# Optimization experiments

Measured on AMD Instinct MI355X. Metric: run time of the kernel, lower is better.

Reference implementation:

```python
import jax, jax.numpy as jnp
import numpy as np

B, L1, D, H = 4, 1024, 512, 16
L, R = 8192, 8
DFF = 4 * D
DH = D // H  # head dim = 32


def _ln(x, g, b, eps=1e-5):
    mu = x.mean(-1, keepdims=True)
    var = ((x - mu) ** 2).mean(-1, keepdims=True)
    return (x - mu) * jax.lax.rsqrt(var + eps) * g + b


def _mha(q_in, k_in, v_in, Wq, bq, Wk, bk, Wv, bv, Wo, bo):
    # Informer FullAttention (mask_flag=False), scale = 1/sqrt(head_dim), mix=False
    Bq, Lq, _ = q_in.shape
    S = k_in.shape[1]
    q = (q_in @ Wq.T + bq).reshape(Bq, Lq, H, DH)
    k = (k_in @ Wk.T + bk).reshape(Bq, S, H, DH)
    v = (v_in @ Wv.T + bv).reshape(Bq, S, H, DH)
    scores = jnp.einsum('blhe,bshe->bhls', q, k) * (1.0 / jnp.sqrt(jnp.float32(DH)))
    A = jax.nn.softmax(scores, axis=-1)
    out = jnp.einsum('bhls,bshd->blhd', A, v).reshape(Bq, Lq, D)
    return out @ Wo.T + bo


def _p(key, *shape):
    return jax.random.normal(key, shape, jnp.float32) * 0.02


def setup_inputs() -> dict:
    ks = jax.random.split(jax.random.key(0), 16)
    inp = {
        'x': jax.random.normal(ks[0], (B, L1, D), jnp.float32),
        'global_feat': jax.random.normal(ks[1], (B, D, L), jnp.float32),
        'conv_w': _p(ks[2], D, D), 'conv_b': jnp.zeros((D,), jnp.float32),
        'sWq': _p(ks[3], D, D), 'sbq': jnp.zeros((D,), jnp.float32),
        'sWk': _p(ks[4], D, D), 'sbk': jnp.zeros((D,), jnp.float32),
        'sWv': _p(ks[5], D, D), 'sbv': jnp.zeros((D,), jnp.float32),
        'sWo': _p(ks[6], D, D), 'sbo': jnp.zeros((D,), jnp.float32),
        'cWq': _p(ks[7], D, D), 'cbq': jnp.zeros((D,), jnp.float32),
        'cWk': _p(ks[8], D, D), 'cbk': jnp.zeros((D,), jnp.float32),
        'cWv': _p(ks[9], D, D), 'cbv': jnp.zeros((D,), jnp.float32),
        'cWo': _p(ks[10], D, D), 'cbo': jnp.zeros((D,), jnp.float32),
        'ffn_w1': _p(ks[11], DFF, D), 'ffn_b1': jnp.zeros((DFF,), jnp.float32),
        'ffn_w2': _p(ks[12], D, DFF), 'ffn_b2': jnp.zeros((D,), jnp.float32),
        'ln1_g': jnp.ones((D,), jnp.float32), 'ln1_b': jnp.zeros((D,), jnp.float32),
        'ln2_g': jnp.ones((D,), jnp.float32), 'ln2_b': jnp.zeros((D,), jnp.float32),
        'ln3_g': jnp.ones((D,), jnp.float32), 'ln3_b': jnp.zeros((D,), jnp.float32),
    }
    return inp


def reference(x, global_feat, conv_w, conv_b,
              sWq, sbq, sWk, sbk, sWv, sbv, sWo, sbo,
              cWq, cbq, cWk, cbk, cWv, cbv, cWo, cbo,
              ffn_w1, ffn_b1, ffn_w2, ffn_b2,
              ln1_g, ln1_b, ln2_g, ln2_b, ln3_g, ln3_b):
    b, c, length = global_feat.shape
    win = 2 * R  # step == window_size -> non-overlapping windows
    nw = (length - win) // win + 1
    w = global_feat[:, :, :nw * win].reshape(b, c, nw, win)
    # norm over singleton last dim == |max - min| per (b, c, window)
    stat = jnp.abs(w.max(-1) - w.min(-1))  # [B, C, NW]
    # pointwise Conv1d(512,512,1) + relu
    res = jax.nn.relu(jnp.einsum('oc,bcn->bon', conv_w, stat) + conv_b[None, :, None])
    cross = res.transpose(0, 2, 1)  # [B, NW, D] tokens for cross attention
    # EncoderLayer3: self-attn -> cross-attn -> FFN, post-LN residuals
    h = _ln(x + _mha(x, x, x, sWq, sbq, sWk, sbk, sWv, sbv, sWo, sbo), ln1_g, ln1_b)
    h = _ln(h + _mha(h, cross, cross, cWq, cbq, cWk, cbk, cWv, cbv, cWo, cbo), ln2_g, ln2_b)
    y = jax.nn.gelu(h @ ffn_w1.T + ffn_b1) @ ffn_w2.T + ffn_b2
    out = _ln(h + y, ln3_g, ln3_b)
    return out.transpose(0, 2, 1)  # [B, D, L1]
```

## Files before the change

### kernel.cpp

```cpp
#include <hip/hip_runtime.h>
#include <stdint.h>
#include <math.h>


typedef short  s16x8 __attribute__((ext_vector_type(8)));
typedef float  f32x4 __attribute__((ext_vector_type(4)));

__device__ inline unsigned short f2bf(float f) {
  uint32_t u = __builtin_bit_cast(uint32_t, f);
  u += 0x7fffu + ((u >> 16) & 1u);
  return (unsigned short)(u >> 16);
}
__device__ inline float bf2f(unsigned short h) {
  uint32_t u = ((uint32_t)h) << 16;
  return __builtin_bit_cast(float, u);
}
__device__ inline uint32_t cvtpk_bf16(float lo, float hi) {
  uint32_t r;
  asm("v_cvt_pk_bf16_f32 %0, %1, %2" : "=v"(r) : "v"(lo), "v"(hi));
  return r;
}

#define QSCALE 0.25503486611627154f

__global__ __launch_bounds__(256) void prep_kernel(
    const float* s0, const float* s1, const float* s2, const float* s3,
    const float* s4, const float* s5, const float* s6, const float* s7,
    const float* s8, const float* s9, const float* s10, const float* s11,
    unsigned short* dst,
    const float* __restrict__ gf, unsigned short* __restrict__ statT,
    const float* __restrict__ sbq, const float* __restrict__ sbk,
    const float* __restrict__ sbv, const float* __restrict__ cbk,
    const float* __restrict__ cbv, float* __restrict__ biasf) {
  const int bid = blockIdx.x;
  const int t = threadIdx.x;
  if (bid < 3200) {
    const size_t cum[13] = {0, 262144, 524288, 786432, 1048576, 1310720,
                            1572864, 1835008, 2097152, 2359296, 3407872,
                            4456448, 6553600};
    const float* srcs[12] = {s0, s1, s2, s3, s4, s5, s6, s7, s8, s9, s10, s11};
    size_t e0 = ((size_t)bid * 256 + t) * 8;
    int seg = 0;
    while (e0 >= cum[seg + 1]) ++seg;
    const float* sp = srcs[seg] + (e0 - cum[seg]);
    float4 a = *(const float4*)sp;
    float4 b = *(const float4*)(sp + 4);
    unsigned short o[8] = {f2bf(a.x), f2bf(a.y), f2bf(a.z), f2bf(a.w),
                           f2bf(b.x), f2bf(b.y), f2bf(b.z), f2bf(b.w)};
    *(uint4*)&dst[e0] = *(const uint4*)o;
  } else if (bid < 7296) {
    int gidx = (bid - 3200) * 256 + t;
    int n = gidx & 511;
    int c = (gidx >> 9) & 511;
    int b = gidx >> 18;
    const float4* p = (const float4*)(gf + ((size_t)(b * 512 + c) << 13) + n * 16);
    float4 w0 = p[0], w1 = p[1], w2 = p[2], w3 = p[3];
    float mx = w0.x, mn = w0.x;
    float vals[15] = {w0.y, w0.z, w0.w, w1.x, w1.y, w1.z, w1.w,
                      w2.x, w2.y, w2.z, w2.w, w3.x, w3.y, w3.z, w3.w};
#pragma unroll
    for (int i = 0; i < 15; ++i) {
      mx = fmaxf(mx, vals[i]);
      mn = fminf(mn, vals[i]);
    }
    statT[((size_t)(b * 512 + n) << 9) + c] = f2bf(mx - mn);
  } else {
    for (int i = t; i < 2560; i += 256) {
      float v;
      if (i < 512) v = sbq[i];
      else if (i < 1024) v = sbk[i - 512];
      else if (i < 1536) v = sbv[i - 1024];
      else if (i < 2048) v = cbk[i - 1536];
      else v = cbv[i - 2048];
      biasf[i] = v;
    }
  }
}

template <int ACT, int OUTBF, int SCALEQ, int BN>
__global__ __launch_bounds__(256) void gemm_bf16(
    const unsigned short* __restrict__ A, const unsigned short* __restrict__ W,
    const float* __restrict__ bias, void* __restrict__ Cout,
    int M, int N, int K) {
  constexpr int NFR = BN / 32;
  __shared__ __align__(16) unsigned short As[2][64 * 64];
  __shared__ __align__(16) unsigned short Bs[2][BN * 64];
  const int t = threadIdx.x;
  const int w = t >> 6, lane = t & 63;
  const int r = lane & 15, g = lane >> 4;
  const int wm = w >> 1, wn = w & 1;
  const int m0 = blockIdx.y * 64, n0 = blockIdx.x * BN;

  auto STAGE = [&](int buf, int k0) {
#pragma unroll
    for (int ii = 0; ii < 2; ++ii) {
      int c = t + 256 * ii;
      int row = c >> 3, sc = c & 7;
      const unsigned short* ga =
          A + (size_t)(m0 + row) * K + k0 + ((sc ^ (row & 7)) << 3);
      __builtin_amdgcn_global_load_lds(
          (const __attribute__((address_space(1))) uint32_t*)ga,
          (__attribute__((address_space(3))) uint32_t*)&As[buf][c * 8], 16, 0, 0);
    }
#pragma unroll
    for (int ii = 0; ii < BN / 32; ++ii) {
      int c = t + 256 * ii;
      int row = c >> 3, sc = c & 7;
      const unsigned short* gb =
          W + (size_t)(n0 + row) * K + k0 + ((sc ^ (row & 7)) << 3);
      __builtin_amdgcn_global_load_lds(
          (const __attribute__((address_space(1))) uint32_t*)gb,
          (__attribute__((address_space(3))) uint32_t*)&Bs[buf][c * 8], 16, 0, 0);
    }
  };

  f32x4 acc[2][NFR];
#pragma unroll
  for (int mi = 0; mi < 2; ++mi)
#pragma unroll
    for (int ni = 0; ni < NFR; ++ni) acc[mi][ni] = (f32x4){0.f, 0.f, 0.f, 0.f};

  STAGE(0, 0);
  __syncthreads();
  int cur = 0;
  for (int k0 = 0; k0 < K; k0 += 64) {
    if (k0 + 64 < K) STAGE(cur ^ 1, k0 + 64);
#pragma unroll
    for (int ks = 0; ks < 2; ++ks) {
      s16x8 af[2], bf[NFR];
#pragma unroll
      for (int mi = 0; mi < 2; ++mi)
        af[mi] = *(const s16x8*)&As[cur][(wm * 32 + mi * 16 + r) * 64 +
                                         (((ks * 4 + g) ^ (r & 7)) << 3)];
#pragma unroll
      for (int ni = 0; ni < NFR; ++ni)
        bf[ni] = *(const s16x8*)&Bs[cur][(wn * (BN / 2) + ni * 16 + r) * 64 +
                                         (((ks * 4 + g) ^ (r & 7)) << 3)];
#pragma unroll
      for (int mi = 0; mi < 2; ++mi)
#pragma unroll
        for (int ni = 0; ni < NFR; ++ni)
          acc[mi][ni] = __builtin_amdgcn_mfma_f32_16x16x32_bf16(
              af[mi], bf[ni], acc[mi][ni], 0, 0, 0);
    }
    __syncthreads();
    cur ^= 1;
  }

#pragma unroll
  for (int ni = 0; ni < NFR; ++ni) {
    const int col = n0 + wn * (BN / 2) + ni * 16 + r;
    const float bv = bias[col];
#pragma unroll
    for (int mi = 0; mi < 2; ++mi) {
#pragma unroll
      for (int rg = 0; rg < 4; ++rg) {
        const int row = m0 + wm * 32 + mi * 16 + g * 4 + rg;
        float v = acc[mi][ni][rg] + bv;
        if (ACT == 1) v = fmaxf(v, 0.f);
        if (ACT == 2) {
          float u = 0.7978845608028654f * (v + 0.044715f * v * v * v);
          float e = __expf(2.f * u);
          float th = 1.f - 2.f / (e + 1.f);
          v = 0.5f * v * (1.f + th);
        }
        if (SCALEQ && col < 512) v *= QSCALE;
        if (OUTBF)
          ((unsigned short*)Cout)[(size_t)row * N + col] = f2bf(v);
        else
          ((float*)Cout)[(size_t)row * N + col] = v;
      }
    }
  }
}

template <int S>
__global__ __launch_bounds__(512) void attn_mfma(
    const unsigned short* __restrict__ Q, int qstride,
    const unsigned short* __restrict__ K, int kstride,
    const unsigned short* __restrict__ V, int vstride,
    unsigned short* __restrict__ O) {
  constexpr int NT = S / 128;
  __shared__ __align__(16) unsigned short Kl[128 * 40];
  __shared__ __align__(16) unsigned short Vl[32 * 136];
  __shared__ __align__(16) unsigned short Pl[8][16 * 136];
  const int t = threadIdx.x;
  const int w = t >> 6, lane = t & 63;
  const int r = lane & 15, g = lane >> 4;
  const int qt = blockIdx.x, h = blockIdx.y, b = blockIdx.z;
  const int q0 = qt * 128 + w * 16;
  const int kvr = t >> 2, dsg = t & 3;

  s16x8 qa = *(const s16x8*)&Q[((size_t)(b * 1024 + q0 + r)) * qstride + h * 32 + g * 8];

  f32x4 o0 = (f32x4){0.f, 0.f, 0.f, 0.f};
  f32x4 o1 = (f32x4){0.f, 0.f, 0.f, 0.f};
  float m = -1e30f, l = 0.f;

  uint4 kA = {}, vA = {}, kB = {}, vB = {};
  auto GLOAD = [&](int nt, uint4& kr, uint4& vr) {
    const int kv0 = nt * 128;
    kr = *(const uint4*)&K[((size_t)(b * S + kv0 + kvr)) * kstride + h * 32 + dsg * 8];
    vr = *(const uint4*)&V[((size_t)(b * S + kv0 + kvr)) * vstride + h * 32 + dsg * 8];
  };
  GLOAD(0, kA, vA);

  for (int nt = 0; nt < NT; ++nt) {
    __syncthreads();
    *(uint4*)&Kl[kvr * 40 + dsg * 8] = kA;
    {
      unsigned short vs[8];
      *(uint4*)vs = vA;
#pragma unroll
      for (int u = 0; u < 8; ++u) Vl[(dsg * 8 + u) * 136 + kvr] = vs[u];
    }
    if (nt + 1 < NT) GLOAD(nt + 1, kB, vB);
    __syncthreads();

    f32x4 s[8];
    __builtin_amdgcn_s_setprio(1);
#pragma unroll
    for (int nb = 0; nb < 8; ++nb) {
      s16x8 ka = *(const s16x8*)&Kl[(nb * 16 + r) * 40 + g * 8];
      s[nb] = __builtin_amdgcn_mfma_f32_16x16x32_bf16(
          ka, qa, (f32x4){0.f, 0.f, 0.f, 0.f}, 0, 0, 0);
    }
    __builtin_amdgcn_s_setprio(0);

    float tm = -1e30f;
#pragma unroll
    for (int nb = 0; nb < 8; ++nb) {
      float a01 = fmaxf(s[nb][0], s[nb][1]);
      float a23 = fmaxf(s[nb][2], s[nb][3]);
      tm = fmaxf(tm, fmaxf(a01, a23));
    }
    tm = fmaxf(tm, __shfl_xor(tm, 16));
    tm = fmaxf(tm, __shfl_xor(tm, 32));
    const float mnew = fmaxf(m, tm);
    const float corr = __builtin_amdgcn_exp2f(m - mnew);
    float ps = 0.f;
#pragma unroll
    for (int nb = 0; nb < 8; ++nb) {
      float p0 = __builtin_amdgcn_exp2f(s[nb][0] - mnew);
      float p1 = __builtin_amdgcn_exp2f(s[nb][1] - mnew);
      float p2 = __builtin_amdgcn_exp2f(s[nb][2] - mnew);
      float p3 = __builtin_amdgcn_exp2f(s[nb][3] - mnew);
      ps += (p0 + p1) + (p2 + p3);
      uint2 pv;
      pv.x = cvtpk_bf16(p0, p1);
      pv.y = cvtpk_bf16(p2, p3);
      *(uint2*)&Pl[w][r * 136 + nb * 16 + g * 4] = pv;
    }
    ps += __shfl_xor(ps, 16);
    ps += __shfl_xor(ps, 32);
    l = l * corr + ps;
    m = mnew;
#pragma unroll
    for (int rg = 0; rg < 4; ++rg) { o0[rg] *= corr; o1[rg] *= corr; }

    __builtin_amdgcn_s_setprio(1);
#pragma unroll
    for (int ks = 0; ks < 4; ++ks) {
      s16x8 va0 = *(const s16x8*)&Vl[r * 136 + ks * 32 + g * 8];
      s16x8 va1 = *(const s16x8*)&Vl[(16 + r) * 136 + ks * 32 + g * 8];
      s16x8 pb  = *(const s16x8*)&Pl[w][r * 136 + ks * 32 + g * 8];
      o0 = __builtin_amdgcn_mfma_f32_16x16x32_bf16(va0, pb, o0, 0, 0, 0);
      o1 = __builtin_amdgcn_mfma_f32_16x16x32_bf16(va1, pb, o1, 0, 0, 0);
    }
    __builtin_amdgcn_s_setprio(0);
    kA = kB; vA = vB;
  }

  const float inv = 1.f / l;
  const size_t row = (size_t)(b * 1024 + q0 + r);
  uint2 w0, w1;
  w0.x = cvtpk_bf16(o0[0] * inv, o0[1] * inv);
  w0.y = cvtpk_bf16(o0[2] * inv, o0[3] * inv);
  w1.x = cvtpk_bf16(o1[0] * inv, o1[1] * inv);
  w1.y = cvtpk_bf16(o1[2] * inv, o1[3] * inv);
  *(uint2*)&O[row * 512 + h * 32 + g * 4]      = w0;
  *(uint2*)&O[row * 512 + h * 32 + 16 + g * 4] = w1;
}

template <int XBF, int ABF>
__global__ __launch_bounds__(256) void ln_kernel(
    const void* __restrict__ X, const void* __restrict__ A,
    const float* __restrict__ gw, const float* __restrict__ bw,
    unsigned short* __restrict__ O) {
  const int rr = blockIdx.x;
  const int t = threadIdx.x;
  const size_t base = (size_t)rr * 512;
  float x0, x1, a0, a1;
  if (XBF) {
    x0 = bf2f(((const unsigned short*)X)[base + t]);
    x1 = bf2f(((const unsigned short*)X)[base + t + 256]);
  } else {
    x0 = ((const float*)X)[base + t];
    x1 = ((const float*)X)[base + t + 256];
  }
  if (ABF) {
    a0 = bf2f(((const unsigned short*)A)[base + t]);
    a1 = bf2f(((const unsigned short*)A)[base + t + 256]);
  } else {
    a0 = ((const float*)A)[base + t];
    a1 = ((const float*)A)[base + t + 256];
  }
  float v0 = x0 + a0;
  float v1 = x1 + a1;
  __shared__ float wsum[4];
  float s = v0 + v1;
#pragma unroll
  for (int of = 32; of; of >>= 1) s += __shfl_down(s, of);
  if ((t & 63) == 0) wsum[t >> 6] = s;
  __syncthreads();
  const float mean = (wsum[0] + wsum[1] + wsum[2] + wsum[3]) * (1.f / 512.f);
  __syncthreads();
  float d0 = v0 - mean, d1 = v1 - mean;
  float s2 = d0 * d0 + d1 * d1;
#pragma unroll
  for (int of = 32; of; of >>= 1) s2 += __shfl_down(s2, of);
  if ((t & 63) == 0) wsum[t >> 6] = s2;
  __syncthreads();
  const float var = (wsum[0] + wsum[1] + wsum[2] + wsum[3]) * (1.f / 512.f);
  const float rstd = rsqrtf(var + 1e-5f);
  O[base + t] = f2bf(d0 * rstd * gw[t] + bw[t]);
  O[base + t + 256] = f2bf(d1 * rstd * gw[t + 256] + bw[t + 256]);
}

__global__ __launch_bounds__(256) void transpose_out_kernel(
    const unsigned short* __restrict__ h3, float* __restrict__ out) {
  __shared__ float tile[64][65];
  const int t = threadIdx.x;
  const int lt = blockIdx.x * 64, ct = blockIdx.y * 64, b = blockIdx.z;
#pragma unroll
  for (int ii = 0; ii < 2; ++ii) {
    int idx = t + 256 * ii;
    int row = idx >> 3, ch = idx & 7;
    uint4 v = *(const uint4*)&h3[((size_t)(b * 1024 + lt + row)) * 512 + ct + ch * 8];
    unsigned short vs[8];
    *(uint4*)vs = v;
#pragma unroll
    for (int u = 0; u < 8; ++u) tile[row][ch * 8 + u] = bf2f(vs[u]);
  }
  __syncthreads();
  const int c = t >> 2, l0 = (t & 3) * 16;
  float* op = &out[((size_t)(b * 512 + ct + c)) * 1024 + lt + l0];
#pragma unroll
  for (int i = 0; i < 4; ++i) {
    float4 o4 = {tile[l0 + i * 4 + 0][c], tile[l0 + i * 4 + 1][c],
                 tile[l0 + i * 4 + 2][c], tile[l0 + i * 4 + 3][c]};
    *(float4*)(op + i * 4) = o4;
  }
}

extern "C" void kernel_launch(void* const* d_in, const int* in_sizes, int n_in,
                              void* d_out, int out_size, void* d_ws, size_t ws_size,
                              hipStream_t stream) {
  const float* x      = (const float*)d_in[0];
  const float* gf     = (const float*)d_in[1];
  const float* conv_w = (const float*)d_in[2];
  const float* conv_b = (const float*)d_in[3];
  const float* sWq = (const float*)d_in[4],  *sbq = (const float*)d_in[5];
  const float* sWk = (const float*)d_in[6],  *sbk = (const float*)d_in[7];
  const float* sWv = (const float*)d_in[8],  *sbv = (const float*)d_in[9];
  const float* sWo = (const float*)d_in[10], *sbo = (const float*)d_in[11];
  const float* cWq = (const float*)d_in[12], *cbq = (const float*)d_in[13];
  const float* cWk = (const float*)d_in[14], *cbk = (const float*)d_in[15];
  const float* cWv = (const float*)d_in[16], *cbv = (const float*)d_in[17];
  const float* cWo = (const float*)d_in[18], *cbo = (const float*)d_in[19];
  const float* fw1 = (const float*)d_in[20], *fb1 = (const float*)d_in[21];
  const float* fw2 = (const float*)d_in[22], *fb2 = (const float*)d_in[23];
  const float* ln1_g = (const float*)d_in[24], *ln1_b = (const float*)d_in[25];
  const float* ln2_g = (const float*)d_in[26], *ln2_b = (const float*)d_in[27];
  const float* ln3_g = (const float*)d_in[28], *ln3_b = (const float*)d_in[29];
  float* out = (float*)d_out;

  unsigned short* bfp = (unsigned short*)d_ws;
  unsigned short* conv_wb = bfp + 0;
  unsigned short* sWqb = bfp + 262144;
  unsigned short* cWqb = bfp + 1310720;
  unsigned short* cWkb = bfp + 1572864;
  unsigned short* cWob = bfp + 2097152;
  unsigned short* sWob = bfp + 1048576;
  unsigned short* fw1b = bfp + 2359296, *fw2b = bfp + 3407872;
  unsigned short* xbf  = bfp + 4456448;

  unsigned short* SC   = bfp + 6553600;
  unsigned short* qkvb = SC;
  unsigned short* ckvb = SC + 6291456;
  unsigned short* qcb  = SC + 8388608;
  unsigned short* ctxb = SC + 12582912;
  unsigned short* projb= SC + 14680064;
  unsigned short* hbf  = SC + 16777216;
  unsigned short* h2bf = SC + 18874368;
  unsigned short* statTb = qcb;
  unsigned short* crossb = ctxb;
  unsigned short* midb   = qkvb;
  float* biasf = (float*)projb;

  prep_kernel<<<7297, 256, 0, stream>>>(
      conv_w, sWq, sWk, sWv, sWo, cWq, cWk, cWv, cWo, fw1, fw2, x, bfp,
      gf, statTb, sbq, sbk, sbv, cbk, cbv, biasf);

  gemm_bf16<1, 1, 0, 64><<<dim3(8, 32), 256, 0, stream>>>(
      statTb, conv_wb, conv_b, crossb, 2048, 512, 512);
  gemm_bf16<0, 1, 1, 128><<<dim3(12, 64), 256, 0, stream>>>(
      xbf, sWqb, biasf, qkvb, 4096, 1536, 512);
  gemm_bf16<0, 1, 0, 64><<<dim3(16, 32), 256, 0, stream>>>(
      crossb, cWkb, biasf + 1536, ckvb, 2048, 1024, 512);

  attn_mfma<1024><<<dim3(8, 16, 4), 512, 0, stream>>>(
      qkvb, 1536, qkvb + 512, 1536, qkvb + 1024, 1536, ctxb);
  gemm_bf16<0, 1, 0, 64><<<dim3(8, 64), 256, 0, stream>>>(
      ctxb, sWob, sbo, projb, 4096, 512, 512);
  ln_kernel<0, 1><<<4096, 256, 0, stream>>>(x, projb, ln1_g, ln1_b, hbf);

  gemm_bf16<0, 1, 1, 64><<<dim3(8, 64), 256, 0, stream>>>(
      hbf, cWqb, cbq, qcb, 4096, 512, 512);
  attn_mfma<512><<<dim3(8, 16, 4), 512, 0, stream>>>(
      qcb, 512, ckvb, 1024, ckvb + 512, 1024, ctxb);
  gemm_bf16<0, 1, 0, 64><<<dim3(8, 64), 256, 0, stream>>>(
      ctxb, cWob, cbo, projb, 4096, 512, 512);
  ln_kernel<1, 1><<<4096, 256, 0, stream>>>(hbf, projb, ln2_g, ln2_b, h2bf);

  gemm_bf16<2, 1, 0, 128><<<dim3(16, 64), 256, 0, stream>>>(
      h2bf, fw1b, fb1, midb, 4096, 2048, 512);
  gemm_bf16<0, 1, 0, 64><<<dim3(8, 64), 256, 0, stream>>>(
      midb, fw2b, fb2, projb, 4096, 512, 2048);
  ln_kernel<1, 1><<<4096, 256, 0, stream>>>(h2bf, projb, ln3_g, ln3_b, hbf);
  transpose_out_kernel<<<dim3(16, 8, 4), 256, 0, stream>>>(hbf, out);
}
```

Baseline: 335.5 us.

## Add 128x128 GEMM tile body and merge conv and QKV GEMM launches

Adds a 128x128-tile bf16 MFMA GEMM body with K-step 32 and double-buffered direct-to-LDS loads. It is used in a new combined kernel that runs the conv projection GEMM and the QKV projection GEMM in one grid by splitting on block index, and also for the FFN first layer. The larger tiles are meant to raise data reuse per block and cut one kernel launch. In exchange there are fewer blocks, which can lower occupancy and leave parts of the GPU idle, and the K-step of 32 means more synchronisations per GEMM.

```diff
diff --git a/kernel.cpp b/kernel.cpp
--- a/kernel.cpp
+++ b/kernel.cpp
@@ -77,6 +77,118 @@
   }
 }
 
+__device__ __forceinline__ void gemm128_body(
+    unsigned short* AsB, unsigned short* BsB,
+    const unsigned short* __restrict__ A, const unsigned short* __restrict__ W,
+    const float* __restrict__ bias, unsigned short* __restrict__ Cout,
+    int M, int N, int K, int m0, int n0, int act, int scaleq) {
+  const int t = threadIdx.x;
+  const int w = t >> 6, lane = t & 63;
+  const int r = lane & 15, g = lane >> 4;
+  const int wm = w >> 1, wn = w & 1;
+
+  auto STAGE = [&](int buf, int k0) {
+    unsigned short* As = AsB + buf * (128 * 32);
+    unsigned short* Bs = BsB + buf * (128 * 32);
+#pragma unroll
+    for (int ii = 0; ii < 2; ++ii) {
+      int c = t + 256 * ii;
+      int row = c >> 2, sc = c & 3;
+      const unsigned short* ga = A + (size_t)(m0 + row) * K + k0 + sc * 8;
+      __builtin_amdgcn_global_load_lds(
+          (const __attribute__((address_space(1))) uint32_t*)ga,
+          (__attribute__((address_space(3))) uint32_t*)&As[c * 8], 16, 0, 0);
+      const unsigned short* gb = W + (size_t)(n0 + row) * K + k0 + sc * 8;
+      __builtin_amdgcn_global_load_lds(
+          (const __attribute__((address_space(1))) uint32_t*)gb,
+          (__attribute__((address_space(3))) uint32_t*)&Bs[c * 8], 16, 0, 0);
+    }
+  };
+
+  f32x4 acc[4][4];
+#pragma unroll
+  for (int mi = 0; mi < 4; ++mi)
+#pragma unroll
+    for (int ni = 0; ni < 4; ++ni) acc[mi][ni] = (f32x4){0.f, 0.f, 0.f, 0.f};
+
+  STAGE(0, 0);
+  __syncthreads();
+  int cur = 0;
+  for (int k0 = 0; k0 < K; k0 += 32) {
+    if (k0 + 32 < K) STAGE(cur ^ 1, k0 + 32);
+    const unsigned short* As = AsB + cur * (128 * 32);
+    const unsigned short* Bs = BsB + cur * (128 * 32);
+    s16x8 af[4], bf[4];
+#pragma unroll
+    for (int mi = 0; mi < 4; ++mi)
+      af[mi] = *(const s16x8*)&As[(wm * 64 + mi * 16 + r) * 32 + g * 8];
+#pragma unroll
+    for (int ni = 0; ni < 4; ++ni)
+      bf[ni] = *(const s16x8*)&Bs[(wn * 64 + ni * 16 + r) * 32 + g * 8];
+#pragma unroll
+    for (int mi = 0; mi < 4; ++mi)
+#pragma unroll
+      for (int ni = 0; ni < 4; ++ni)
+        acc[mi][ni] = __builtin_amdgcn_mfma_f32_16x16x32_bf16(
+            af[mi], bf[ni], acc[mi][ni], 0, 0, 0);
+    __syncthreads();
+    cur ^= 1;
+  }
+
+#pragma unroll
+  for (int ni = 0; ni < 4; ++ni) {
+    const int col = n0 + wn * 64 + ni * 16 + r;
+    const float bv = bias[col];
+#pragma unroll
+    for (int mi = 0; mi < 4; ++mi) {
+#pragma unroll
+      for (int rg = 0; rg < 4; ++rg) {
+        const int row = m0 + wm * 64 + mi * 16 + g * 4 + rg;
+        float v = acc[mi][ni][rg] + bv;
+        if (act == 1) v = fmaxf(v, 0.f);
+        if (act == 2) {
+          float u = 0.7978845608028654f * (v + 0.044715f * v * v * v);
+          float e = __expf(2.f * u);
+          float th = 1.f - 2.f / (e + 1.f);
+          v = 0.5f * v * (1.f + th);
+        }
+        if (scaleq && col < 512) v *= QSCALE;
+        Cout[(size_t)row * N + col] = f2bf(v);
+      }
+    }
+  }
+}
+
+__global__ __launch_bounds__(256) void gemm_conv_qkv(
+    const unsigned short* __restrict__ statT,
+    const unsigned short* __restrict__ convW, const float* __restrict__ convB,
+    unsigned short* __restrict__ cross,
+    const unsigned short* __restrict__ xbf,
+    const unsigned short* __restrict__ qkvW, const float* __restrict__ qkvBias,
+    unsigned short* __restrict__ qkv) {
+  __shared__ __align__(16) unsigned short As[2 * 128 * 32];
+  __shared__ __align__(16) unsigned short Bs[2 * 128 * 32];
+  const int bid = blockIdx.x;
+  if (bid < 64) {
+    gemm128_body(As, Bs, statT, convW, convB, cross, 2048, 512, 512,
+                 (bid >> 2) * 128, (bid & 3) * 128, 1, 0);
+  } else {
+    const int b2 = bid - 64;
+    gemm128_body(As, Bs, xbf, qkvW, qkvBias, qkv, 4096, 1536, 512,
+                 (b2 / 12) * 128, (b2 % 12) * 128, 0, 1);
+  }
+}
+
+__global__ __launch_bounds__(256) void gemm128_kernel(
+    const unsigned short* __restrict__ A, const unsigned short* __restrict__ W,
+    const float* __restrict__ bias, unsigned short* __restrict__ C,
+    int M, int N, int K, int act) {
+  __shared__ __align__(16) unsigned short As[2 * 128 * 32];
+  __shared__ __align__(16) unsigned short Bs[2 * 128 * 32];
+  gemm128_body(As, Bs, A, W, bias, C, M, N, K,
+               blockIdx.y * 128, blockIdx.x * 128, act, 0);
+}
+
 template <int ACT, int OUTBF, int SCALEQ, int BN>
 __global__ __launch_bounds__(256) void gemm_bf16(
     const unsigned short* __restrict__ A, const unsigned short* __restrict__ W,
@@ -402,10 +514,9 @@
       conv_w, sWq, sWk, sWv, sWo, cWq, cWk, cWv, cWo, fw1, fw2, x, bfp,
       gf, statTb, sbq, sbk, sbv, cbk, cbv, biasf);
 
-  gemm_bf16<1, 1, 0, 64><<<dim3(8, 32), 256, 0, stream>>>(
-      statTb, conv_wb, conv_b, crossb, 2048, 512, 512);
-  gemm_bf16<0, 1, 1, 128><<<dim3(12, 64), 256, 0, stream>>>(
-      xbf, sWqb, biasf, qkvb, 4096, 1536, 512);
+  gemm_conv_qkv<<<448, 256, 0, stream>>>(
+      statTb, conv_wb, conv_b, crossb, xbf, sWqb, biasf, qkvb);
+
   gemm_bf16<0, 1, 0, 64><<<dim3(16, 32), 256, 0, stream>>>(
       crossb, cWkb, biasf + 1536, ckvb, 2048, 1024, 512);
 
@@ -423,8 +534,8 @@
       ctxb, cWob, cbo, projb, 4096, 512, 512);
   ln_kernel<1, 1><<<4096, 256, 0, stream>>>(hbf, projb, ln2_g, ln2_b, h2bf);
 
-  gemm_bf16<2, 1, 0, 128><<<dim3(16, 64), 256, 0, stream>>>(
-      h2bf, fw1b, fb1, midb, 4096, 2048, 512);
+  gemm128_kernel<<<dim3(16, 32), 256, 0, stream>>>(
+      h2bf, fw1b, fb1, midb, 4096, 2048, 512, 2);
   gemm_bf16<0, 1, 0, 64><<<dim3(8, 64), 256, 0, stream>>>(
       midb, fw2b, fb2, projb, 4096, 512, 2048);
   ln_kernel<1, 1><<<4096, 256, 0, stream>>>(h2bf, projb, ln3_g, ln3_b, hbf);
```

Measured after the change: 330.9 us. About the same (-1.4%).
